# Kernel optimization log

Measured on AMD Instinct MI355X. Metric: run time of the kernel, lower is better.

## Reference

```python
import jax, jax.numpy as jnp
import numpy as np

B, T, D, H, K, V, F = 4, 4096, 1024, 8, 128, 128, 4096
EPS = 1e-5


def setup_inputs() -> dict:
    key = jax.random.key(0)
    ks = jax.random.split(key, 12)
    s = 0.02
    return {
        "x": jax.random.normal(ks[0], (B, T, D), jnp.float32),
        "Wq": jax.random.normal(ks[1], (D, H * K), jnp.float32) * s,
        "Wk": jax.random.normal(ks[2], (D, H * K), jnp.float32) * s,
        "Wv": jax.random.normal(ks[3], (D, H * V), jnp.float32) * s,
        "Wb": jax.random.normal(ks[4], (D, H), jnp.float32) * s,
        "Wa": jax.random.normal(ks[5], (D, H), jnp.float32) * s,
        "Wo": jax.random.normal(ks[6], (H * V, D), jnp.float32) * s,
        "ln1_w": jnp.ones((D,), jnp.float32),
        "ln1_b": jnp.zeros((D,), jnp.float32),
        "ln2_w": jnp.ones((D,), jnp.float32),
        "ln2_b": jnp.zeros((D,), jnp.float32),
        "W1": jax.random.normal(ks[7], (D, F), jnp.float32) * s,
        "b1": jnp.zeros((F,), jnp.float32),
        "W2": jax.random.normal(ks[8], (F, D), jnp.float32) * s,
        "b2": jnp.zeros((D,), jnp.float32),
    }


def layernorm(x, w, b):
    m = jnp.mean(x, -1, keepdims=True)
    v = jnp.var(x, -1, keepdims=True)
    return (x - m) * jax.lax.rsqrt(v + EPS) * w + b


def l2norm(x):
    return x * jax.lax.rsqrt(jnp.sum(x * x, -1, keepdims=True) + 1e-6)


def gdn_recurrence(q, k, v, alpha, beta):
    """Delta rule: S_t = a_t (I - b_t k k^T) S_{t-1} + b_t v k^T ; o_t = S_t^T q_t.
    q,k: [B,T,H,K]; v: [B,T,H,V]; alpha,beta: [B,T,H]. Returns o: [B,T,H,V]."""
    qT = jnp.moveaxis(q, 1, 0)  # [T,B,H,K]
    kT = jnp.moveaxis(k, 1, 0)
    vT = jnp.moveaxis(v, 1, 0)  # [T,B,H,V]
    aT = jnp.moveaxis(alpha, 1, 0)  # [T,B,H]
    bT = jnp.moveaxis(beta, 1, 0)

    def step(S, inp):  # S: [B,H,K,V]
        q_t, k_t, v_t, a_t, b_t = inp
        kS = jnp.einsum("bhk,bhkv->bhv", k_t, S)  # k^T S
        bk = (b_t[..., None] * k_t)[..., :, None]  # [B,H,K,1]
        S = a_t[..., None, None] * (S - bk * kS[..., None, :]) + bk * v_t[..., None, :]
        o = jnp.einsum("bhk,bhkv->bhv", q_t, S)
        return S, o

    S0 = jnp.zeros((q.shape[0], H, K, V), q.dtype)
    _, oT = jax.lax.scan(step, S0, (qT, kT, vT, aT, bT))
    return jnp.moveaxis(oT, 0, 1)  # [B,T,H,V]


def reference(x, Wq, Wk, Wv, Wb, Wa, Wo, ln1_w, ln1_b, ln2_w, ln2_b, W1, b1, W2, b2):
    b, t, _ = x.shape
    n = layernorm(x, ln1_w, ln1_b)
    q = l2norm(jax.nn.silu(n @ Wq).reshape(b, t, H, K))
    k = l2norm(jax.nn.silu(n @ Wk).reshape(b, t, H, K))
    v = jax.nn.silu(n @ Wv).reshape(b, t, H, V)
    beta = jax.nn.sigmoid(n @ Wb)   # [B,T,H]
    alpha = jax.nn.sigmoid(n @ Wa)  # gated decay in (0,1)
    o = gdn_recurrence(q, k, v, alpha, beta).reshape(b, t, H * V) @ Wo
    x = x + o
    h = layernorm(x, ln2_w, ln2_b)
    x = x + (jax.nn.gelu(h @ W1 + b1, approximate=False) @ W2 + b2)
    return x
```

## Files before the change

### kernel.cpp

```cpp
#include <hip/hip_runtime.h>
#include <stdint.h>

#define B_ 4
#define T_ 4096
#define D_ 1024
#define H_ 8
#define K_ 128
#define V_ 128
#define F_ 4096
#define N_TOK (B_*T_)

typedef unsigned short u16;
typedef __attribute__((ext_vector_type(8))) short bf16x8;
typedef __attribute__((ext_vector_type(4))) float f32x4;

__device__ __forceinline__ float bf2f(u16 u){
  unsigned x = ((unsigned)u) << 16;
  return __builtin_bit_cast(float, x);
}
__device__ __forceinline__ u16 f2bf(float f){
  unsigned x = __builtin_bit_cast(unsigned, f);
  x += 0x7FFFu + ((x >> 16) & 1u);
  return (u16)(x >> 16);
}

__global__ void transpose_k(const float* __restrict__ in, u16* __restrict__ out, int R, int C){
  __shared__ u16 tile[32][33];
  int c0 = blockIdx.x*32, r0 = blockIdx.y*32;
  int tx = threadIdx.x, ty = threadIdx.y;
  #pragma unroll
  for (int i = ty; i < 32; i += 8)
    tile[i][tx] = f2bf(in[(size_t)(r0+i)*C + c0 + tx]);
  __syncthreads();
  #pragma unroll
  for (int i = ty; i < 32; i += 8)
    out[(size_t)(c0+i)*R + r0 + tx] = tile[tx][i];
}

template<bool F32IN>
__global__ __launch_bounds__(256) void ln_k(const void* __restrict__ xv, const float* __restrict__ w,
                                            const float* __restrict__ bias, u16* __restrict__ out){
  __shared__ float ssh[4], qsh[4];
  int row = blockIdx.x; int t = threadIdx.x;
  float v0,v1,v2,v3;
  if constexpr (F32IN){
    const float* x = (const float*)xv;
    float4 r = ((const float4*)(x + (size_t)row*D_))[t];
    v0=r.x; v1=r.y; v2=r.z; v3=r.w;
  } else {
    const u16* x = (const u16*)xv;
    ushort4 r = ((const ushort4*)(x + (size_t)row*D_))[t];
    v0=bf2f(r.x); v1=bf2f(r.y); v2=bf2f(r.z); v3=bf2f(r.w);
  }
  float s = v0+v1+v2+v3;
  float q = v0*v0+v1*v1+v2*v2+v3*v3;
  #pragma unroll
  for (int m=1;m<64;m<<=1){ s += __shfl_xor(s,m); q += __shfl_xor(q,m); }
  int wave = t>>6, lane = t&63;
  if (lane==0){ ssh[wave]=s; qsh[wave]=q; }
  __syncthreads();
  s = ssh[0]+ssh[1]+ssh[2]+ssh[3];
  q = qsh[0]+qsh[1]+qsh[2]+qsh[3];
  float mean = s * (1.0f/D_);
  float var  = q * (1.0f/D_) - mean*mean;
  float inv  = rsqrtf(var + 1e-5f);
  float4 wr = ((const float4*)w)[t];
  float4 br = ((const float4*)bias)[t];
  ushort4 o;
  o.x = f2bf((v0-mean)*inv*wr.x + br.x);
  o.y = f2bf((v1-mean)*inv*wr.y + br.y);
  o.z = f2bf((v2-mean)*inv*wr.z + br.z);
  o.w = f2bf((v3-mean)*inv*wr.w + br.w);
  ((ushort4*)(out + (size_t)row*D_))[t] = o;
}

template<int EPI, bool F32OUT>
__global__ __launch_bounds__(256,1)
void gemm_k(const u16* __restrict__ A, const u16* __restrict__ Bt, void* __restrict__ Cptr,
            int M, int N, int K,
            const float* __restrict__ fres, const u16* __restrict__ bres,
            const float* __restrict__ bias){
  __shared__ alignas(16) u16 As[128*32];
  __shared__ alignas(16) u16 Bs[128*32];
  int t = threadIdx.x;
  int wave = t>>6, lane = t&63;
  int lm = lane & 15, lq = lane >> 4;
  int m0 = blockIdx.y*128, n0 = blockIdx.x*128;
  int wm = (wave&1)*64, wn = (wave>>1)*64;

  const u16* Ag = A  + (size_t)(m0 + (t>>2))*K + (t&3)*8;
  const u16* Bg = Bt + (size_t)(n0 + (t>>2))*K + (t&3)*8;
  const size_t rstride = (size_t)64*K;

  f32x4 acc[4][4];
  #pragma unroll
  for (int i=0;i<4;i++)
    #pragma unroll
    for (int j=0;j<4;j++){ acc[i][j].x=0.f; acc[i][j].y=0.f; acc[i][j].z=0.f; acc[i][j].w=0.f; }

  uint4 ra0, ra1, rb0, rb1;
  auto loadRegs = [&](int kt){
    const u16* a = Ag + kt*32;
    const u16* b = Bg + kt*32;
    ra0 = *(const uint4*)a;             ra1 = *(const uint4*)(a + rstride);
    rb0 = *(const uint4*)b;             rb1 = *(const uint4*)(b + rstride);
  };
  loadRegs(0);

  u16* wA = As + t*8;
  u16* wB = Bs + t*8;
  const u16* rA = As + (size_t)(wm + lm)*32 + lq*8;
  const u16* rB = Bs + (size_t)(wn + lm)*32 + lq*8;

  int nk = K >> 5;
  for (int kt=0; kt<nk; ++kt){
    __syncthreads();
    *(uint4*)wA = ra0; *(uint4*)(wA+2048) = ra1;
    *(uint4*)wB = rb0; *(uint4*)(wB+2048) = rb1;
    __syncthreads();
    if (kt+1 < nk) loadRegs(kt+1);
    bf16x8 af[4], bfr[4];
    #pragma unroll
    for (int i=0;i<4;i++){
      af[i]  = *(const bf16x8*)(rA + i*16*32);
      bfr[i] = *(const bf16x8*)(rB + i*16*32);
    }
    #pragma unroll
    for (int i=0;i<4;i++)
      #pragma unroll
      for (int j=0;j<4;j++)
        acc[i][j] = __builtin_amdgcn_mfma_f32_16x16x32_bf16(af[i], bfr[j], acc[i][j], 0,0,0);
  }

  #pragma unroll
  for (int i=0;i<4;i++){
    int rbase = m0 + wm + i*16 + lq*4;
    #pragma unroll
    for (int j=0;j<4;j++){
      int col = n0 + wn + j*16 + lm;
      #pragma unroll
      for (int r=0;r<4;r++){
        float v = acc[i][j][r];
        size_t idx = (size_t)(rbase + r)*N + col;
        if (EPI==1) v += fres[idx];
        if (EPI==2){ v += bias[col]; v = 0.5f*v*(1.0f+erff(v*0.70710678118f)); }
        if (EPI==3){ v += bias[col] + bf2f(bres[idx]); }
        if constexpr (F32OUT) ((float*)Cptr)[idx] = v;
        else                  ((u16*)Cptr)[idx]  = f2bf(v);
      }
    }
  }
}

__global__ __launch_bounds__(256) void wab_pack(const float* __restrict__ Wb, const float* __restrict__ Wa,
                                                u16* __restrict__ wabT){
  int g = blockIdx.x*256 + threadIdx.x;
  int j = g >> 10, d = g & 1023;
  const float* W = (j < 8) ? Wb : Wa;
  wabT[g] = f2bf(W[(size_t)d*H_ + (j&7)]);
}

__global__ __launch_bounds__(256) void ab_k(const u16* __restrict__ n, const u16* __restrict__ wabT,
                                            float* __restrict__ beta, float* __restrict__ alpha){
  int tid = threadIdx.x, lane = tid&63, wv = tid>>6;
  int lm = lane & 15, lq = lane >> 4;
  int tok0 = (blockIdx.x*4 + wv)*16;
  const u16* np = n + (size_t)(tok0 + lm)*D_;
  const u16* wp = wabT + (size_t)lm*D_;
  f32x4 acc = {0.f,0.f,0.f,0.f};
  #pragma unroll
  for (int kt=0; kt<32; ++kt){
    bf16x8 af = *(const bf16x8*)(np + kt*32 + lq*8);
    bf16x8 bf = *(const bf16x8*)(wp + kt*32 + lq*8);
    acc = __builtin_amdgcn_mfma_f32_16x16x32_bf16(af, bf, acc, 0,0,0);
  }
  #pragma unroll
  for (int r=0;r<4;r++){
    int tok = tok0 + lq*4 + r;
    float sg = 1.f/(1.f+expf(-acc[r]));
    if (lm < 8) beta [(size_t)tok*H_ + lm]     = sg;
    else        alpha[(size_t)tok*H_ + lm - 8] = sg;
  }
}

__global__ __launch_bounds__(128) void act_k(u16* __restrict__ qkv){
  __shared__ float tot[2];
  int y = blockIdx.y;
  int tok = blockIdx.x >> 3, head = blockIdx.x & 7;
  u16* p = qkv + (size_t)y*((size_t)N_TOK*D_) + (size_t)tok*D_ + head*K_ + threadIdx.x;
  float xv = bf2f(*p);
  float s = xv / (1.f + expf(-xv));
  if (y < 2){
    float sq = s*s;
    #pragma unroll
    for (int m=1;m<64;m<<=1) sq += __shfl_xor(sq,m);
    int wave = threadIdx.x >> 6;
    if ((threadIdx.x&63)==0) tot[wave]=sq;
    __syncthreads();
    s *= rsqrtf(tot[0]+tot[1] + 1e-6f);
  }
  *p = f2bf(s);
}

__global__ __launch_bounds__(256) void gdn_pre(const u16* __restrict__ k, const u16* __restrict__ q,
        const float* __restrict__ alpha, const float* __restrict__ beta,
        u16* __restrict__ T_all, u16* __restrict__ Att_all, float* __restrict__ cumg_all){
  __shared__ alignas(16) char sm[49664];
  u16*   Ks = (u16*)sm;
  u16*   Qs = (u16*)(sm+16384);
  float* Tl = (float*)(sm+16384);
  float* Ml = (float*)(sm+32768);
  float* cg = (float*)(sm+49152);
  float* bv = (float*)(sm+49408);
  int c = blockIdx.x, bh = blockIdx.y;
  int b = bh>>3, h = bh&7;
  int tid = threadIdx.x, lane = tid&63, wv = tid>>6;
  int q4 = lane>>4, n = lane&15;
  size_t rowbase = ((size_t)b*T_ + c*64);
  const u16* kg = k + rowbase*D_ + h*K_;
  const u16* qg = q + rowbase*D_ + h*K_;
  #pragma unroll
  for (int i=0;i<4;i++){
    int g = tid + i*256; int s = g>>4; int k8 = (g&15)*8;
    *(uint4*)&Ks[s*128+k8] = *(const uint4*)(kg + (size_t)s*D_ + k8);
    *(uint4*)&Qs[s*128+k8] = *(const uint4*)(qg + (size_t)s*D_ + k8);
  }
  if (tid < 64){
    float a = alpha[(rowbase+tid)*H_ + h];
    bv[tid] = beta[(rowbase+tid)*H_ + h];
    float xx = a;
    #pragma unroll
    for (int d=1; d<64; d<<=1){
      float y = __shfl_up(xx, (unsigned)d);
      if (tid >= d) xx *= y;
    }
    cg[tid] = xx;
    cumg_all[((size_t)c*32+bh)*64 + tid] = xx;
  }
  __syncthreads();
  f32x4 kk[4], qk[4];
  #pragma unroll
  for (int nb=0; nb<4; nb++){
    f32x4 a1={0,0,0,0}, a2={0,0,0,0};
    #pragma unroll
    for (int ks=0; ks<4; ks++){
      bf16x8 af = *(const bf16x8*)&Ks[(16*wv+n)*128 + ks*32 + q4*8];
      bf16x8 qf = *(const bf16x8*)&Qs[(16*wv+n)*128 + ks*32 + q4*8];
      bf16x8 bf = *(const bf16x8*)&Ks[(16*nb+n)*128 + ks*32 + q4*8];
      a1 = __builtin_amdgcn_mfma_f32_16x16x32_bf16(af, bf, a1, 0,0,0);
      a2 = __builtin_amdgcn_mfma_f32_16x16x32_bf16(qf, bf, a2, 0,0,0);
    }
    kk[nb]=a1; qk[nb]=a2;
  }
  __syncthreads();
  size_t gbase = ((size_t)c*32+bh)*4096;
  #pragma unroll
  for (int nb=0; nb<4; nb++){
    #pragma unroll
    for (int r=0;r<4;r++){
      int srow = 16*wv + 4*q4 + r;
      int scol = 16*nb + n;
      float m = 0.f, at = 0.f;
      if (scol <= srow){
        float rb = (cg[srow]/cg[scol]) * bv[scol];
        at = rb * qk[nb][r];
        if (scol < srow) m = rb * kk[nb][r];
      }
      Ml[srow*64 + scol] = m;
      Att_all[gbase + srow*64 + scol] = f2bf(at);
    }
  }
  #pragma unroll
  for (int i=0;i<16;i++){
    int g = tid + i*256;
    Tl[g] = ((g>>6) == (g&63)) ? 1.f : 0.f;
  }
  __syncthreads();
  if (tid < 64){
    int j = tid;
    for (int s=1; s<64; ++s){
      float acc = 0.f;
      for (int r=0; r<s; ++r)
        acc += Ml[s*64+r] * Tl[r*64+j];
      Tl[s*64+j] -= acc;
    }
  }
  __syncthreads();
  #pragma unroll
  for (int i=0;i<16;i++){
    int g = tid + i*256;
    T_all[gbase + g] = f2bf(Tl[g]);
  }
}

__global__ __launch_bounds__(256,1) void gdn_scan(const u16* __restrict__ q, const u16* __restrict__ k,
        const u16* __restrict__ v, const float* __restrict__ beta,
        const u16* __restrict__ T_all, const u16* __restrict__ Att_all,
        const float* __restrict__ cumg_all, u16* __restrict__ o){
  __shared__ alignas(16) char sm[64000];
  u16* Kt  = (u16*)sm;
  u16* Ts  = (u16*)(sm+18432);
  u16* As_ = (u16*)(sm+27648);
  u16* Sbt = (u16*)(sm+36864);
  u16* RUt = (u16*)(sm+54272);
  float* cg = (float*)(sm+63488);
  float* bv = (float*)(sm+63744);
  int bh = blockIdx.x, half = blockIdx.y;
  int b = bh>>3, h = bh&7;
  int tid = threadIdx.x, lane = tid&63, wv = tid>>6;
  int q4 = lane>>4, n = lane&15;
  int colb = half*64 + wv*16;
  f32x4 Sa[8];
  #pragma unroll
  for (int i=0;i<8;i++) Sa[i] = (f32x4){0.f,0.f,0.f,0.f};

  for (int c=0; c<64; ++c){
    size_t rowbase = ((size_t)b*T_ + c*64);
    const u16* kg = k + rowbase*D_ + h*K_;
    const u16* qg = q + rowbase*D_ + h*K_;
    #pragma unroll
    for (int i=0;i<4;i++){
      int g = tid + i*256; int s = g>>4; int k8 = (g&15)*8;
      uint4 u = *(const uint4*)(kg + (size_t)s*D_ + k8);
      u16 tmp[8]; *(uint4*)tmp = u;
      #pragma unroll
      for (int j=0;j<8;j++) Kt[(k8+j)*72 + s] = tmp[j];
    }
    {
      size_t tb = ((size_t)c*32+bh)*4096;
      #pragma unroll
      for (int i=0;i<2;i++){
        int g = tid+i*256; int r = g>>3; int c8=(g&7)*8;
        *(uint4*)&Ts[r*72+c8]  = *(const uint4*)(T_all  + tb + r*64 + c8);
        *(uint4*)&As_[r*72+c8] = *(const uint4*)(Att_all + tb + r*64 + c8);
      }
      if (tid<64){
        cg[tid] = cumg_all[((size_t)c*32+bh)*64 + tid];
        bv[tid] = beta[(rowbase+tid)*H_ + h];
      }
    }
    float vreg[16];
    const u16* vg = v + rowbase*D_ + h*V_ + colb + n;
    #pragma unroll
    for (int mb=0; mb<4; mb++)
      #pragma unroll
      for (int r=0;r<4;r++)
        vreg[mb*4+r] = bf2f(vg[(size_t)(16*mb+4*q4+r)*D_]);
    #pragma unroll
    for (int mb=0; mb<8; mb++){
      ushort4 w4;
      w4.x=f2bf(Sa[mb][0]); w4.y=f2bf(Sa[mb][1]); w4.z=f2bf(Sa[mb][2]); w4.w=f2bf(Sa[mb][3]);
      *(ushort4*)&Sbt[(wv*16+n)*136 + mb*16 + q4*4] = w4;
    }
    __syncthreads();
    f32x4 Pa[4], Oqa[4];
    #pragma unroll
    for (int mb=0; mb<4; mb++){
      f32x4 p={0,0,0,0}, oq={0,0,0,0};
      #pragma unroll
      for (int ks=0; ks<4; ks++){
        bf16x8 ak = *(const bf16x8*)(kg + (size_t)(16*mb+n)*D_ + ks*32 + q4*8);
        bf16x8 aq = *(const bf16x8*)(qg + (size_t)(16*mb+n)*D_ + ks*32 + q4*8);
        bf16x8 bs = *(const bf16x8*)&Sbt[(wv*16+n)*136 + ks*32 + q4*8];
        p  = __builtin_amdgcn_mfma_f32_16x16x32_bf16(ak, bs, p, 0,0,0);
        oq = __builtin_amdgcn_mfma_f32_16x16x32_bf16(aq, bs, oq, 0,0,0);
      }
      Pa[mb]=p; Oqa[mb]=oq;
    }
    #pragma unroll
    for (int mb=0; mb<4; mb++){
      ushort4 w4;
      #pragma unroll
      for (int r=0;r<4;r++){
        int t = 16*mb+4*q4+r;
        ((u16*)&w4)[r] = f2bf(vreg[mb*4+r] - cg[t]*Pa[mb][r]);
      }
      *(ushort4*)&RUt[(wv*16+n)*72 + mb*16 + q4*4] = w4;
    }
    f32x4 Ua[4];
    #pragma unroll
    for (int mb=0; mb<4; mb++){
      f32x4 u={0,0,0,0};
      #pragma unroll
      for (int ks=0; ks<2; ks++){
        bf16x8 at = *(const bf16x8*)&Ts[(16*mb+n)*72 + ks*32 + q4*8];
        bf16x8 br = *(const bf16x8*)&RUt[(wv*16+n)*72 + ks*32 + q4*8];
        u = __builtin_amdgcn_mfma_f32_16x16x32_bf16(at, br, u, 0,0,0);
      }
      Ua[mb]=u;
    }
    #pragma unroll
    for (int mb=0; mb<4; mb++){
      ushort4 w4;
      #pragma unroll
      for (int r=0;r<4;r++) ((u16*)&w4)[r] = f2bf(Ua[mb][r]);
      *(ushort4*)&RUt[(wv*16+n)*72 + mb*16 + q4*4] = w4;
    }
    u16* og = o + rowbase*D_ + h*V_ + colb + n;
    #pragma unroll
    for (int mb=0; mb<4; mb++){
      f32x4 oa={0,0,0,0};
      #pragma unroll
      for (int ks=0; ks<2; ks++){
        bf16x8 aa = *(const bf16x8*)&As_[(16*mb+n)*72 + ks*32 + q4*8];
        bf16x8 bu = *(const bf16x8*)&RUt[(wv*16+n)*72 + ks*32 + q4*8];
        oa = __builtin_amdgcn_mfma_f32_16x16x32_bf16(aa, bu, oa, 0,0,0);
      }
      #pragma unroll
      for (int r=0;r<4;r++){
        int t = 16*mb+4*q4+r;
        og[(size_t)t*D_] = f2bf(cg[t]*Oqa[mb][r] + oa[r]);
      }
    }
    float gC = cg[63];
    #pragma unroll
    for (int mb=0; mb<4; mb++){
      ushort4 w4;
      #pragma unroll
      for (int r=0;r<4;r++){
        int t = 16*mb+4*q4+r;
        ((u16*)&w4)[r] = f2bf((gC/cg[t])*bv[t]*Ua[mb][r]);
      }
      *(ushort4*)&RUt[(wv*16+n)*72 + mb*16 + q4*4] = w4;
    }
    #pragma unroll
    for (int mb=0; mb<8; mb++){
      f32x4 s = Sa[mb]*gC;
      #pragma unroll
      for (int ks=0; ks<2; ks++){
        bf16x8 akt = *(const bf16x8*)&Kt[(16*mb+n)*72 + ks*32 + q4*8];
        bf16x8 bu  = *(const bf16x8*)&RUt[(wv*16+n)*72 + ks*32 + q4*8];
        s = __builtin_amdgcn_mfma_f32_16x16x32_bf16(akt, bu, s, 0,0,0);
      }
      Sa[mb]=s;
    }
    __syncthreads();
  }
}

extern "C" void kernel_launch(void* const* d_in, const int* in_sizes, int n_in,
                              void* d_out, int out_size, void* d_ws, size_t ws_size,
                              hipStream_t stream){
  const float* x    = (const float*)d_in[0];
  const float* Wq   = (const float*)d_in[1];
  const float* Wk   = (const float*)d_in[2];
  const float* Wv   = (const float*)d_in[3];
  const float* Wb   = (const float*)d_in[4];
  const float* Wa   = (const float*)d_in[5];
  const float* Wo   = (const float*)d_in[6];
  const float* ln1w = (const float*)d_in[7];
  const float* ln1b = (const float*)d_in[8];
  const float* ln2w = (const float*)d_in[9];
  const float* ln2b = (const float*)d_in[10];
  const float* W1   = (const float*)d_in[11];
  const float* b1   = (const float*)d_in[12];
  const float* W2   = (const float*)d_in[13];
  const float* b2   = (const float*)d_in[14];

  char* ws = (char*)d_ws;
  size_t off = 0;
  auto alloc = [&](size_t bytes)->char*{
    char* p = ws + off; off += (bytes + 255) & ~(size_t)255; return p;
  };
  u16* WqT = (u16*)alloc((size_t)1024*1024*2);
  u16* WkT = (u16*)alloc((size_t)1024*1024*2);
  u16* WvT = (u16*)alloc((size_t)1024*1024*2);
  u16* WoT = (u16*)alloc((size_t)1024*1024*2);
  u16* W1T = (u16*)alloc((size_t)4096*1024*2);
  u16* W2T = (u16*)alloc((size_t)1024*4096*2);
  u16* wabT = (u16*)alloc((size_t)16*1024*2);
  float* alphaB = (float*)alloc((size_t)N_TOK*H_*4);
  float* betaB  = (float*)alloc((size_t)N_TOK*H_*4);
  u16* x1 = (u16*)alloc((size_t)N_TOK*D_*2);
  u16* n1 = (u16*)alloc((size_t)N_TOK*D_*2);
  u16* qb = (u16*)alloc((size_t)N_TOK*D_*2);
  u16* kb = (u16*)alloc((size_t)N_TOK*D_*2);
  u16* vb = (u16*)alloc((size_t)N_TOK*D_*2);
  u16* ob = (u16*)alloc((size_t)N_TOK*D_*2);
  u16* ffa = qb;
  if (ws_size < off) return;

  u16*   T_all   = n1;
  u16*   Att_all = n1 + (size_t)2048*4096;
  float* cumg    = (float*)x1;

  dim3 tb(32,8);
  transpose_k<<<dim3(32,32),  tb, 0, stream>>>(Wq, WqT, 1024, 1024);
  transpose_k<<<dim3(32,32),  tb, 0, stream>>>(Wk, WkT, 1024, 1024);
  transpose_k<<<dim3(32,32),  tb, 0, stream>>>(Wv, WvT, 1024, 1024);
  transpose_k<<<dim3(32,32),  tb, 0, stream>>>(Wo, WoT, 1024, 1024);
  transpose_k<<<dim3(128,32), tb, 0, stream>>>(W1, W1T, 1024, 4096);
  transpose_k<<<dim3(32,128), tb, 0, stream>>>(W2, W2T, 4096, 1024);
  wab_pack<<<64, 256, 0, stream>>>(Wb, Wa, wabT);

  ln_k<true><<<N_TOK, 256, 0, stream>>>(x, ln1w, ln1b, n1);

  gemm_k<0,false><<<dim3(8,128), 256, 0, stream>>>(n1, WqT, qb, N_TOK, 1024, 1024, nullptr, nullptr, nullptr);
  gemm_k<0,false><<<dim3(8,128), 256, 0, stream>>>(n1, WkT, kb, N_TOK, 1024, 1024, nullptr, nullptr, nullptr);
  gemm_k<0,false><<<dim3(8,128), 256, 0, stream>>>(n1, WvT, vb, N_TOK, 1024, 1024, nullptr, nullptr, nullptr);
  ab_k<<<256, 256, 0, stream>>>(n1, wabT, betaB, alphaB);
  act_k<<<dim3(N_TOK*H_, 3), 128, 0, stream>>>(qb);

  gdn_pre <<<dim3(64,32), 256, 0, stream>>>(kb, qb, alphaB, betaB, T_all, Att_all, cumg);
  gdn_scan<<<dim3(32,2),  256, 0, stream>>>(qb, kb, vb, betaB, T_all, Att_all, cumg, ob);

  gemm_k<1,false><<<dim3(8,128), 256, 0, stream>>>(ob, WoT, x1, N_TOK, 1024, 1024, x, nullptr, nullptr);
  ln_k<false><<<N_TOK, 256, 0, stream>>>(x1, ln2w, ln2b, n1);
  gemm_k<2,false><<<dim3(32,128), 256, 0, stream>>>(n1, W1T, ffa, N_TOK, 4096, 1024, nullptr, nullptr, b1);
  gemm_k<3,true><<<dim3(8,128), 256, 0, stream>>>(ffa, W2T, d_out, N_TOK, 1024, 4096, nullptr, x1, b2);
}
```

Before: 1.548 ms.

## Prefetch next chunk into registers and swizzle K transpose stores in recurrence kernel

The chunked delta-rule recurrence kernel now loads the next chunk's K, T, Att, V, cumulative gate and beta into registers right after the barrier, so global latency overlaps the current chunk's MFMA work. The K transpose into LDS now pairs tokens with a lane shuffle so each thread writes 32-bit words. It also applies a rotation swizzle to cut LDS bank conflicts, and the matching reads are rotated the same way. This costs more registers per thread, which may lower occupancy or cause spills.

```diff
diff --git a/kernel.cpp b/kernel.cpp
--- a/kernel.cpp
+++ b/kernel.cpp
@@ -314,38 +314,79 @@
   #pragma unroll
   for (int i=0;i<8;i++) Sa[i] = (f32x4){0.f,0.f,0.f,0.f};
 
+  uint4 kv[4], tv[2], av[2];
+  u16 vvv[16];
+  float cgr = 0.f, bvr = 0.f;
+
+  auto prefetch = [&](int c){
+    size_t rowbase = ((size_t)b*T_ + c*64);
+    const u16* kg = k + rowbase*D_ + h*K_;
+    #pragma unroll
+    for (int i=0;i<4;i++){
+      int g = tid + i*256; int s = g>>4; int k8 = (g&15)*8;
+      kv[i] = *(const uint4*)(kg + (size_t)s*D_ + k8);
+    }
+    size_t tb = ((size_t)c*32+bh)*4096;
+    #pragma unroll
+    for (int i=0;i<2;i++){
+      int g = tid+i*256; int r = g>>3; int c8=(g&7)*8;
+      tv[i] = *(const uint4*)(T_all  + tb + r*64 + c8);
+      av[i] = *(const uint4*)(Att_all + tb + r*64 + c8);
+    }
+    const u16* vg = v + rowbase*D_ + h*V_ + colb + n;
+    #pragma unroll
+    for (int mb=0; mb<4; mb++)
+      #pragma unroll
+      for (int r=0;r<4;r++)
+        vvv[mb*4+r] = vg[(size_t)(16*mb+4*q4+r)*D_];
+    if (tid < 64){
+      cgr = cumg_all[((size_t)c*32+bh)*64 + tid];
+      bvr = beta[(rowbase+tid)*H_ + h];
+    }
+  };
+
+  prefetch(0);
+
   for (int c=0; c<64; ++c){
     size_t rowbase = ((size_t)b*T_ + c*64);
     const u16* kg = k + rowbase*D_ + h*K_;
     const u16* qg = q + rowbase*D_ + h*K_;
+
     #pragma unroll
     for (int i=0;i<4;i++){
-      int g = tid + i*256; int s = g>>4; int k8 = (g&15)*8;
-      uint4 u = *(const uint4*)(kg + (size_t)s*D_ + k8);
-      u16 tmp[8]; *(uint4*)tmp = u;
-      #pragma unroll
-      for (int j=0;j<8;j++) Kt[(k8+j)*72 + s] = tmp[j];
-    }
-    {
-      size_t tb = ((size_t)c*32+bh)*4096;
-      #pragma unroll
-      for (int i=0;i<2;i++){
-        int g = tid+i*256; int r = g>>3; int c8=(g&7)*8;
-        *(uint4*)&Ts[r*72+c8]  = *(const uint4*)(T_all  + tb + r*64 + c8);
-        *(uint4*)&As_[r*72+c8] = *(const uint4*)(Att_all + tb + r*64 + c8);
-      }
-      if (tid<64){
-        cg[tid] = cumg_all[((size_t)c*32+bh)*64 + tid];
-        bv[tid] = beta[(rowbase+tid)*H_ + h];
-      }
-    }
+      int g = tid + i*256; int s = g>>4; int kb8 = (g&15)*8;
+      uint4 pv;
+      pv.x = (unsigned)__shfl_xor((int)kv[i].x, 16);
+      pv.y = (unsigned)__shfl_xor((int)kv[i].y, 16);
+      pv.z = (unsigned)__shfl_xor((int)kv[i].z, 16);
+      pv.w = (unsigned)__shfl_xor((int)kv[i].w, 16);
+      int odd = s & 1;
+      int t0  = s & ~1;
+      int jb  = odd ? 4 : 0;
+      int rot = (8*(g&15)) & 63;
+      const u16* own = (const u16*)&kv[i];
+      const u16* par = (const u16*)&pv;
+      #pragma unroll
+      for (int j=0;j<4;j++){
+        int jj = jb + j;
+        unsigned lo = odd ? par[jj] : own[jj];
+        unsigned hi = odd ? own[jj] : par[jj];
+        int addr = (kb8+jj)*72 + ((t0 + rot) & 63);
+        *(unsigned*)&Kt[addr] = lo | (hi << 16);
+      }
+    }
+    #pragma unroll
+    for (int i=0;i<2;i++){
+      int g = tid+i*256; int r = g>>3; int c8=(g&7)*8;
+      *(uint4*)&Ts[r*72+c8]  = tv[i];
+      *(uint4*)&As_[r*72+c8] = av[i];
+    }
+    if (tid < 64){ cg[tid] = cgr; bv[tid] = bvr; }
+
     float vreg[16];
-    const u16* vg = v + rowbase*D_ + h*V_ + colb + n;
-    #pragma unroll
-    for (int mb=0; mb<4; mb++)
-      #pragma unroll
-      for (int r=0;r<4;r++)
-        vreg[mb*4+r] = bf2f(vg[(size_t)(16*mb+4*q4+r)*D_]);
+    #pragma unroll
+    for (int i=0;i<16;i++) vreg[i] = bf2f(vvv[i]);
+
     #pragma unroll
     for (int mb=0; mb<8; mb++){
       ushort4 w4;
@@ -353,6 +394,9 @@
       *(ushort4*)&Sbt[(wv*16+n)*136 + mb*16 + q4*4] = w4;
     }
     __syncthreads();
+
+    if (c+1 < 64) prefetch(c+1);
+
     f32x4 Pa[4], Oqa[4];
     #pragma unroll
     for (int mb=0; mb<4; mb++){
@@ -426,9 +470,12 @@
     #pragma unroll
     for (int mb=0; mb<8; mb++){
       f32x4 s = Sa[mb]*gC;
+      int krow = 16*mb + n;
+      int rot  = (16*mb + 8*(n>>3)) & 63;
       #pragma unroll
       for (int ks=0; ks<2; ks++){
-        bf16x8 akt = *(const bf16x8*)&Kt[(16*mb+n)*72 + ks*32 + q4*8];
+        int tt = (ks*32 + q4*8 + rot) & 63;
+        bf16x8 akt = *(const bf16x8*)&Kt[krow*72 + tt];
         bf16x8 bu  = *(const bf16x8*)&RUt[(wv*16+n)*72 + ks*32 + q4*8];
         s = __builtin_amdgcn_mfma_f32_16x16x32_bf16(akt, bu, s, 0,0,0);
       }
```

Result: slower. 1.599 ms (+3.3%).
